# Kernel optimization log

Measured on AMD Instinct MI355X. Metric: run time of the kernel, lower is better.

## Reference

```python
import jax, jax.numpy as jnp
import numpy as np

EMBEDDING_DIM = 512
HEAD_DIM = 64
B, T_NEW, T_CACHE = 8, 1024, 3072
T_TOTAL = T_NEW + T_CACHE


def setup_inputs() -> dict:
    key = jax.random.key(0)
    ks = jax.random.split(key, 6)
    x = jax.random.normal(ks[0], (B, T_NEW, EMBEDDING_DIM), dtype=jnp.float32)
    cache_k = jax.random.normal(ks[1], (B, T_CACHE, HEAD_DIM), dtype=jnp.float32)
    cache_v = jax.random.normal(ks[2], (B, T_CACHE, HEAD_DIM), dtype=jnp.float32)
    # Causal mask rows for the new tokens: cache fully visible, causal among new.
    # Equivalent to tril(ones(T_TOTAL, T_TOTAL))[T_CACHE:, :].
    rows = jnp.arange(T_NEW)[:, None] + T_CACHE  # absolute positions of new tokens
    cols = jnp.arange(T_TOTAL)[None, :]
    mask = (cols <= rows).astype(jnp.int32)  # [T_NEW, T_TOTAL]
    scale = 1.0 / np.sqrt(EMBEDDING_DIM)
    Wq = jax.random.normal(ks[3], (EMBEDDING_DIM, HEAD_DIM), dtype=jnp.float32) * scale
    Wk = jax.random.normal(ks[4], (EMBEDDING_DIM, HEAD_DIM), dtype=jnp.float32) * scale
    Wv = jax.random.normal(ks[5], (EMBEDDING_DIM, HEAD_DIM), dtype=jnp.float32) * scale
    return {"x": x, "mask": mask, "cache_k": cache_k, "cache_v": cache_v,
            "Wq": Wq, "Wk": Wk, "Wv": Wv}


def reference(x, mask, cache_k, cache_v, Wq, Wk, Wv):
    # Projections (nn.Linear with bias=False)
    q = jnp.einsum("btc,cd->btd", x, Wq)  # [B, T_new, D]
    k_new = jnp.einsum("btc,cd->btd", x, Wk)
    v_new = jnp.einsum("btc,cd->btd", x, Wv)
    k = jnp.concatenate([cache_k, k_new], axis=1)  # [B, T_total, D]
    v = jnp.concatenate([cache_v, v_new], axis=1)
    d = k.shape[-1]
    scores = jnp.einsum("btd,bsd->bts", q, k) * (d ** -0.5)  # [B, T_new, T_total]
    T = q.shape[1]
    cur_mask = mask[:T, :k.shape[1]]  # [T_new, T_total]
    scores = jnp.where(cur_mask == 0, jnp.float32(-jnp.inf), scores)
    probs = jax.nn.softmax(scores, axis=-1)
    # Dropout is identity in eval mode (deterministic reference).
    out = jnp.einsum("bts,bsd->btd", probs, v)  # [B, T_new, D]
    return out, k, v
```

## Files before the change

kernel.cpp:

```cpp
#include <hip/hip_runtime.h>

#define NB     8
#define TNEW   1024
#define TCACHE 3072
#define TTOT   4096
#define EMB    512
#define HD     64

typedef __bf16 bf16x8 __attribute__((ext_vector_type(8)));
typedef __bf16 bf16x4 __attribute__((ext_vector_type(4)));
typedef float  f32x4  __attribute__((ext_vector_type(4)));

#define MFMA(a,b,c) __builtin_amdgcn_mfma_f32_16x16x32_bf16((a),(b),(c),0,0,0)

#define GLOAD_LDS16(g, l) \
    __builtin_amdgcn_global_load_lds((const __attribute__((address_space(1))) void*)(g), \
                                     (__attribute__((address_space(3))) void*)(l), 16, 0, 0)

#define QSCALE 0.180336880f

#define WS_WT   0
#define WS_KBF  196608
#define WS_VTB  4390912
#define WS_OP   8585216
#define WS_ML   16973824


__global__ __launch_bounds__(256) void prep(const float* __restrict__ ck,
                                            const float* __restrict__ cv,
                                            const float* __restrict__ Wq,
                                            const float* __restrict__ Wk,
                                            const float* __restrict__ Wv,
                                            float* __restrict__ kout,
                                            float* __restrict__ vout,
                                            __bf16* __restrict__ kb,
                                            __bf16* __restrict__ vtb,
                                            __bf16* __restrict__ wt) {
    __shared__ __bf16 vl[64][72];
    const int blk = blockIdx.x;
    const int tid = threadIdx.x;
    if (blk < 768) {
#pragma unroll
        for (int it = 0; it < 2; ++it) {
            const int i = blk * 256 + tid + it * 196608;
            const int b = i / 49152;
            const int f = i - b * 49152;
            const int s = f >> 4, d = (f & 15) * 4;
            const float4 kd = ((const float4*)ck)[i];
            ((float4*)(kout + (size_t)b * TTOT * HD))[f] = kd;
            bf16x4 k4;
            k4[0] = (__bf16)kd.x; k4[1] = (__bf16)kd.y;
            k4[2] = (__bf16)kd.z; k4[3] = (__bf16)kd.w;
            *(bf16x4*)(kb + (size_t)b * TTOT * HD + s * HD + d) = k4;
        }
    } else if (blk < 1152) {
        const int tb = blk - 768;
        const int b = tb / 48, si = tb - (tb / 48) * 48;
        const int sbase = si * 64;
        const float4* src = (const float4*)(cv + ((size_t)b * TCACHE + sbase) * HD);
        float4* dstf = (float4*)(vout + ((size_t)b * TTOT + sbase) * HD);
#pragma unroll
        for (int k = 0; k < 4; ++k) {
            const int f = tid + 256 * k;
            const int s = f >> 4, d4 = (f & 15) * 4;
            const float4 v = src[f];
            dstf[f] = v;
            bf16x4 t;
            t[0] = (__bf16)v.x; t[1] = (__bf16)v.y;
            t[2] = (__bf16)v.z; t[3] = (__bf16)v.w;
            *(bf16x4*)&vl[s][d4] = t;
        }
        __syncthreads();
        const int d = tid >> 2, sc = tid & 3;
        bf16x8 o0, o1;
#pragma unroll
        for (int i = 0; i < 8; ++i) {
            o0[i] = vl[sc * 16 + i][d];
            o1[i] = vl[sc * 16 + 8 + i][d];
        }
        __bf16* vt = vtb + ((size_t)b * HD + d) * TTOT + sbase + sc * 16;
        *(bf16x8*)vt = o0;
        *(bf16x8*)(vt + 8) = o1;
    } else {
        const int tb = blk - 1152;
        const int m = tb >> 3;
        const int ct = (tb & 7) * 64;
        const float* W = (m == 0) ? Wq : (m == 1) ? Wk : Wv;
        const float4* src = (const float4*)(W + (size_t)ct * HD);
#pragma unroll
        for (int k = 0; k < 4; ++k) {
            const int f = tid + 256 * k;
            const int c = f >> 4, d4 = (f & 15) * 4;
            const float4 v = src[f];
            bf16x4 t;
            t[0] = (__bf16)v.x; t[1] = (__bf16)v.y;
            t[2] = (__bf16)v.z; t[3] = (__bf16)v.w;
            *(bf16x4*)&vl[c][d4] = t;
        }
        __syncthreads();
        const int d = tid >> 2, sc = tid & 3;
        bf16x8 o0, o1;
#pragma unroll
        for (int i = 0; i < 8; ++i) {
            o0[i] = vl[sc * 16 + i][d];
            o1[i] = vl[sc * 16 + 8 + i][d];
        }
        __bf16* wr = wt + (size_t)m * HD * EMB + (size_t)d * EMB + ct + sc * 16;
        *(bf16x8*)wr = o0;
        *(bf16x8*)(wr + 8) = o1;
    }
}

__global__ __launch_bounds__(128) void proj_mfma(const float* __restrict__ x,
                                                 const __bf16* __restrict__ wt,
                                                 __bf16* __restrict__ qb,
                                                 float* __restrict__ kout,
                                                 float* __restrict__ vout,
                                                 __bf16* __restrict__ kb,
                                                 __bf16* __restrict__ vtb) {
    __shared__ __bf16 xs[32][520];
    __shared__ __bf16 vls[2][64][24];
    const int tid = threadIdx.x;
    const int w = tid >> 6, lane = tid & 63;
    const int lo = lane & 15, hi = lane >> 4;
    const int r0 = blockIdx.x * 32 + w * 16;
    const int b = r0 >> 10;
    const int t0r = r0 & (TNEW - 1);

    {
        const float4* xg = (const float4*)(x + (size_t)blockIdx.x * 32 * EMB);
#pragma unroll
        for (int k = 0; k < 32; ++k) {
            const int f = tid + 128 * k;
            const int row = f >> 7, col4 = (f & 127) * 4;
            const float4 v = xg[f];
            bf16x4 t;
            t[0] = (__bf16)v.x; t[1] = (__bf16)v.y;
            t[2] = (__bf16)v.z; t[3] = (__bf16)v.w;
            *(bf16x4*)&xs[row][col4] = t;
        }
    }
    __syncthreads();

    for (int m = 0; m < 3; ++m) {
        const __bf16* wm = wt + (size_t)m * HD * EMB;
        f32x4 acc[4];
#pragma unroll
        for (int n = 0; n < 4; ++n) acc[n] = (f32x4){0.f, 0.f, 0.f, 0.f};
#pragma unroll
        for (int c = 0; c < 16; ++c) {
            const bf16x8 ax = *(const bf16x8*)&xs[w * 16 + lo][c * 32 + hi * 8];
#pragma unroll
            for (int n = 0; n < 4; ++n) {
                const bf16x8 bw = *(const bf16x8*)(wm + (size_t)(n * 16 + lo) * EMB + c * 32 + hi * 8);
                acc[n] = MFMA(ax, bw, acc[n]);
            }
        }
#pragma unroll
        for (int n = 0; n < 4; ++n) {
#pragma unroll
            for (int rr = 0; rr < 4; ++rr) {
                const int grow = r0 + hi * 4 + rr;
                const int t = grow & (TNEW - 1);
                const int d = n * 16 + lo;
                const float val = acc[n][rr];
                if (m == 0) {
                    qb[(size_t)grow * HD + d] = (__bf16)(val * QSCALE);
                } else if (m == 1) {
                    const size_t kv = ((size_t)b * TTOT + TCACHE + t) * HD + d;
                    kout[kv] = val;
                    kb[kv] = (__bf16)val;
                } else {
                    const size_t kv = ((size_t)b * TTOT + TCACHE + t) * HD + d;
                    vout[kv] = val;
                    vls[w][d][hi * 4 + rr] = (__bf16)val;
                }
            }
        }
    }
    __syncthreads();
    bf16x8 v0 = *(const bf16x8*)&vls[w][lane][0];
    bf16x8 v1 = *(const bf16x8*)&vls[w][lane][8];
    __bf16* vt = vtb + ((size_t)b * HD + lane) * TTOT + TCACHE + t0r;
    *(bf16x8*)vt = v0;
    *(bf16x8*)(vt + 8) = v1;
}

#define QB 128
#define NSPLIT 8
__global__ __launch_bounds__(512, 4) void attn_mfma(const __bf16* __restrict__ qb,
                                                    const __bf16* __restrict__ kb,
                                                    const __bf16* __restrict__ vtb,
                                                    __bf16* __restrict__ Opart,
                                                    float* __restrict__ mlpart) {
    __shared__ __align__(16) __bf16 Kt[3][64 * 64];
    __shared__ __align__(16) __bf16 Vts[3][64 * 64];
    __shared__ __align__(16) __bf16 P_lds[8][16][72];

    const int tid = threadIdx.x;
    const int wv = tid >> 6, lane = tid & 63;
    const int lo = lane & 15, hi = lane >> 4;

    const int bid = blockIdx.x;
    const int b = bid & 7;
    const int idx = bid >> 3;
    const int split = idx & 7;
    const int qloc = idx >> 3;
    const int t0 = qloc * QB;
    const int row0 = b * TNEW + t0;

    const int ntiles = (TCACHE + t0 + QB) >> 6;
    const int count = (ntiles - split + 7) >> 3;

    const __bf16* Kb = kb + (size_t)b * TTOT * HD;
    const __bf16* Vb = vtb + (size_t)b * HD * TTOT;

    const int r_sub = lane >> 3;
    const int row_st = wv * 8 + r_sub;
    const int c_st = ((lane & 7) * 16) ^ (r_sub << 4);

#define STAGE(s, bi) do { \
        const char* gk_ = (const char*)Kb + (size_t)((s) + row_st) * 128 + c_st; \
        const char* gv_ = (const char*)Vb + ((size_t)row_st * TTOT + (s)) * 2 + c_st; \
        GLOAD_LDS16(gk_, Kt[bi] + row_st * 64); \
        GLOAD_LDS16(gv_, Vts[bi] + row_st * 64); \
    } while (0)

    const int t0w = t0 + wv * 16;
    const __bf16* Qw = qb + (size_t)(row0 + wv * 16) * HD;
    const bf16x8 aq0 = *(const bf16x8*)(Qw + (size_t)lo * HD + hi * 8);
    const bf16x8 aq1 = *(const bf16x8*)(Qw + (size_t)lo * HD + 32 + hi * 8);

    f32x4 o[4];
    float mg = -1e30f, lg = 0.f;
#pragma unroll
    for (int n = 0; n < 4; ++n) o[n] = (f32x4){0.f, 0.f, 0.f, 0.f};

    STAGE(split * 64, 0);
    if (count > 1) {
        STAGE(split * 64 + 512, 1);
        asm volatile("s_waitcnt vmcnt(2)" ::: "memory");
    } else {
        asm volatile("s_waitcnt vmcnt(0)" ::: "memory");
    }
    __builtin_amdgcn_s_barrier();
    __builtin_amdgcn_sched_barrier(0);

    const int sw = (lo & 7) << 3;

    int s0 = split * 64;
    int buf = 0;
    for (int it = 0; it < count; ++it, s0 += NSPLIT * 64) {
        const __bf16* Kl = Kt[buf];
        const __bf16* Vl = Vts[buf];

        bf16x8 bk[4][2], bv[4][2];
#pragma unroll
        for (int kg = 0; kg < 4; ++kg) {
            const int kr = (kg * 16 + lo) * 64;
            bk[kg][0] = *(const bf16x8*)(Kl + kr + ((hi * 8) ^ sw));
            bk[kg][1] = *(const bf16x8*)(Kl + kr + ((32 + hi * 8) ^ sw));
        }
#pragma unroll
        for (int n = 0; n < 4; ++n) {
            const int vr = (n * 16 + lo) * 64;
            bv[n][0] = *(const bf16x8*)(Vl + vr + ((hi * 8) ^ sw));
            bv[n][1] = *(const bf16x8*)(Vl + vr + ((32 + hi * 8) ^ sw));
        }

        const f32x4 z = (f32x4){0.f, 0.f, 0.f, 0.f};
        f32x4 sc[4];
#pragma unroll
        for (int kg = 0; kg < 4; ++kg) {
            sc[kg] = MFMA(bk[kg][0], aq0, z);
            sc[kg] = MFMA(bk[kg][1], aq1, sc[kg]);
        }

        if (s0 + 63 > TCACHE + t0w) {
            const int lim = TCACHE + t0w + lo;
#pragma unroll
            for (int kg = 0; kg < 4; ++kg)
#pragma unroll
                for (int rr = 0; rr < 4; ++rr)
                    if (s0 + kg * 16 + hi * 4 + rr > lim) sc[kg][rr] = -1e30f;
        }

        f32x4 mx = sc[0];
        mx = (f32x4){fmaxf(mx[0], sc[1][0]), fmaxf(mx[1], sc[1][1]),
                     fmaxf(mx[2], sc[1][2]), fmaxf(mx[3], sc[1][3])};
        mx = (f32x4){fmaxf(mx[0], sc[2][0]), fmaxf(mx[1], sc[2][1]),
                     fmaxf(mx[2], sc[2][2]), fmaxf(mx[3], sc[2][3])};
        mx = (f32x4){fmaxf(mx[0], sc[3][0]), fmaxf(mx[1], sc[3][1]),
                     fmaxf(mx[2], sc[3][2]), fmaxf(mx[3], sc[3][3])};
        float mt = fmaxf(fmaxf(mx[0], mx[1]), fmaxf(mx[2], mx[3]));
        mt = fmaxf(mt, __shfl_xor(mt, 16));
        mt = fmaxf(mt, __shfl_xor(mt, 32));

        if (__any(mt > mg + 8.0f)) {
            const float mn = fmaxf(mg, mt);
            const float corr = exp2f(mg - mn);
            lg *= corr;
            mg = mn;
            float cb[4];
#pragma unroll
            for (int rr = 0; rr < 4; ++rr) cb[rr] = __shfl(corr, hi * 4 + rr);
#pragma unroll
            for (int n = 0; n < 4; ++n)
#pragma unroll
                for (int rr = 0; rr < 4; ++rr) o[n][rr] *= cb[rr];
        }

        float ps = 0.f;
#pragma unroll
        for (int kg = 0; kg < 4; ++kg) {
            const float e0 = exp2f(sc[kg][0] - mg);
            const float e1 = exp2f(sc[kg][1] - mg);
            const float e2 = exp2f(sc[kg][2] - mg);
            const float e3 = exp2f(sc[kg][3] - mg);
            ps += (e0 + e1) + (e2 + e3);
            bf16x4 pk;
            pk[0] = (__bf16)e0; pk[1] = (__bf16)e1;
            pk[2] = (__bf16)e2; pk[3] = (__bf16)e3;
            *(bf16x4*)&P_lds[wv][lo][kg * 16 + hi * 4] = pk;
        }
        ps += __shfl_xor(ps, 16);
        ps += __shfl_xor(ps, 32);
        lg += ps;
        asm volatile("" ::: "memory");

        const bf16x8 ap0 = *(const bf16x8*)&P_lds[wv][lo][hi * 8];
        const bf16x8 ap1 = *(const bf16x8*)&P_lds[wv][lo][32 + hi * 8];
#pragma unroll
        for (int n = 0; n < 4; ++n) o[n] = MFMA(ap0, bv[n][0], o[n]);
#pragma unroll
        for (int n = 0; n < 4; ++n) o[n] = MFMA(ap1, bv[n][1], o[n]);
        asm volatile("" ::: "memory");

        if (it + 2 < count) {
            int nb = buf + 2; if (nb >= 3) nb -= 3;
            STAGE(s0 + 2 * NSPLIT * 64, nb);
        }
        if (it + 1 < count) {
            if (it + 2 < count) { asm volatile("s_waitcnt vmcnt(2)" ::: "memory"); }
            else                { asm volatile("s_waitcnt vmcnt(0)" ::: "memory"); }
            __builtin_amdgcn_s_barrier();
            __builtin_amdgcn_sched_barrier(0);
        }
        buf = (buf == 2) ? 0 : buf + 1;
    }
#undef STAGE

    __bf16* Ow = Opart + ((size_t)split * (NB * TNEW) + row0 + wv * 16) * HD;
#pragma unroll
    for (int n = 0; n < 4; ++n)
#pragma unroll
        for (int rr = 0; rr < 4; ++rr)
            Ow[(size_t)(hi * 4 + rr) * HD + n * 16 + lo] = (__bf16)o[n][rr];
    if (hi == 0) {
        float* mlw = mlpart + ((size_t)split * (NB * TNEW) + row0 + wv * 16) * 2;
        mlw[lo * 2]     = mg;
        mlw[lo * 2 + 1] = lg;
    }
}

__global__ __launch_bounds__(256) void combine(const __bf16* __restrict__ Opart,
                                               const float* __restrict__ mlpart,
                                               float* __restrict__ out) {
    const int e = blockIdx.x * 256 + threadIdx.x;
    const int lane = threadIdx.x & 63;
    const int row = e >> 6, d = e & 63;
    const float2 ml2 = *(const float2*)&mlpart[(((size_t)(lane & 7)) * (NB * TNEW) + row) * 2];
    float mf = -1e30f;
#pragma unroll
    for (int s = 0; s < NSPLIT; ++s) mf = fmaxf(mf, __shfl(ml2.x, s));
    float lf = 0.f, acc = 0.f;
#pragma unroll
    for (int s = 0; s < NSPLIT; ++s) {
        const float ms = __shfl(ml2.x, s);
        const float ls = __shfl(ml2.y, s);
        const float f = exp2f(ms - mf);
        lf += ls * f;
        acc += (float)Opart[((size_t)s * (NB * TNEW) + row) * HD + d] * f;
    }
    out[e] = acc / lf;
}

extern "C" void kernel_launch(void* const* d_in, const int* in_sizes, int n_in,
                              void* d_out, int out_size, void* d_ws, size_t ws_size,
                              hipStream_t stream) {
    (void)in_sizes; (void)n_in; (void)out_size; (void)ws_size;
    const float* x  = (const float*)d_in[0];
    const float* ck = (const float*)d_in[2];
    const float* cv = (const float*)d_in[3];
    const float* Wq = (const float*)d_in[4];
    const float* Wk = (const float*)d_in[5];
    const float* Wv = (const float*)d_in[6];

    float* out  = (float*)d_out;
    float* kout = out + (size_t)NB * TNEW * HD;
    float* vout = kout + (size_t)NB * TTOT * HD;

    char* ws = (char*)d_ws;
    __bf16* wt  = (__bf16*)(ws + WS_WT);
    __bf16* kbf = (__bf16*)(ws + WS_KBF);
    __bf16* vtb = (__bf16*)(ws + WS_VTB);
    __bf16* Op  = (__bf16*)(ws + WS_OP);
    float*  ml  = (float*)(ws + WS_ML);
    __bf16* qb  = (__bf16*)d_out;

    prep<<<dim3(1176), dim3(256), 0, stream>>>(ck, cv, Wq, Wk, Wv, kout, vout, kbf, vtb, wt);
    proj_mfma<<<dim3(256), dim3(128), 0, stream>>>(x, wt, qb, kout, vout, kbf, vtb);
    attn_mfma<<<dim3(512), dim3(512), 0, stream>>>(qb, kbf, vtb, Op, ml);
    combine<<<dim3(2048), dim3(256), 0, stream>>>(Op, ml, out);
}
```

Measured before the change: 50.09 us.

## Keep P in registers by permuting V^T token layout; raise attention occupancy

The V^T buffer is now written with a permuted token order within each 64-token tile. This lets the exponentiated scores from the QK MFMA output be packed directly into the A operand of the PV MFMA, with no round trip through LDS. The P_lds buffer and its stores and loads are removed. K and V fragments are now loaded just before use instead of all up front, and launch bounds rise to 6 waves per SIMD, which should lower register pressure and raise occupancy. The risks are the narrower 8-byte V^T stores, possible spills under the tighter register budget, and correctness depending on the K-dimension permutation matching exactly.

Result: no change. 50.39 us (+0.6%).

```diff
diff --git a/kernel.cpp b/kernel.cpp
--- a/kernel.cpp
+++ b/kernel.cpp
@@ -72,15 +72,14 @@
         }
         __syncthreads();
         const int d = tid >> 2, sc = tid & 3;
-        bf16x8 o0, o1;
-#pragma unroll
-        for (int i = 0; i < 8; ++i) {
-            o0[i] = vl[sc * 16 + i][d];
-            o1[i] = vl[sc * 16 + 8 + i][d];
-        }
-        __bf16* vt = vtb + ((size_t)b * HD + d) * TTOT + sbase + sc * 16;
-        *(bf16x8*)vt = o0;
-        *(bf16x8*)(vt + 8) = o1;
+        __bf16* vt = vtb + ((size_t)b * HD + d) * TTOT + sbase + (sc >> 1) * 32 + (sc & 1) * 4;
+#pragma unroll
+        for (int t4 = 0; t4 < 4; ++t4) {
+            bf16x4 o;
+#pragma unroll
+            for (int c = 0; c < 4; ++c) o[c] = vl[sc * 16 + t4 * 4 + c][d];
+            *(bf16x4*)(vt + t4 * 8) = o;
+        }
     } else {
         const int tb = blk - 1152;
         const int m = tb >> 3;
@@ -179,23 +178,29 @@
         }
     }
     __syncthreads();
-    bf16x8 v0 = *(const bf16x8*)&vls[w][lane][0];
-    bf16x8 v1 = *(const bf16x8*)&vls[w][lane][8];
-    __bf16* vt = vtb + ((size_t)b * HD + lane) * TTOT + TCACHE + t0r;
-    *(bf16x8*)vt = v0;
-    *(bf16x8*)(vt + 8) = v1;
+    {
+        const int tb4 = TCACHE + (t0r & ~63);
+        const int m4 = (t0r >> 4) & 3;
+        __bf16* vt = vtb + ((size_t)b * HD + lane) * TTOT + tb4 + (m4 >> 1) * 32 + (m4 & 1) * 4;
+#pragma unroll
+        for (int t4 = 0; t4 < 4; ++t4) {
+            bf16x4 o;
+#pragma unroll
+            for (int c = 0; c < 4; ++c) o[c] = vls[w][lane][t4 * 4 + c];
+            *(bf16x4*)(vt + t4 * 8) = o;
+        }
+    }
 }
 
 #define QB 128
 #define NSPLIT 8
-__global__ __launch_bounds__(512, 4) void attn_mfma(const __bf16* __restrict__ qb,
+__global__ __launch_bounds__(512, 6) void attn_mfma(const __bf16* __restrict__ qb,
                                                     const __bf16* __restrict__ kb,
                                                     const __bf16* __restrict__ vtb,
                                                     __bf16* __restrict__ Opart,
                                                     float* __restrict__ mlpart) {
     __shared__ __align__(16) __bf16 Kt[3][64 * 64];
     __shared__ __align__(16) __bf16 Vts[3][64 * 64];
-    __shared__ __align__(16) __bf16 P_lds[8][16][72];
 
     const int tid = threadIdx.x;
     const int wv = tid >> 6, lane = tid & 63;
@@ -254,26 +259,15 @@
         const __bf16* Kl = Kt[buf];
         const __bf16* Vl = Vts[buf];
 
-        bf16x8 bk[4][2], bv[4][2];
+        const f32x4 z = (f32x4){0.f, 0.f, 0.f, 0.f};
+        f32x4 sc[4];
 #pragma unroll
         for (int kg = 0; kg < 4; ++kg) {
             const int kr = (kg * 16 + lo) * 64;
-            bk[kg][0] = *(const bf16x8*)(Kl + kr + ((hi * 8) ^ sw));
-            bk[kg][1] = *(const bf16x8*)(Kl + kr + ((32 + hi * 8) ^ sw));
-        }
-#pragma unroll
-        for (int n = 0; n < 4; ++n) {
-            const int vr = (n * 16 + lo) * 64;
-            bv[n][0] = *(const bf16x8*)(Vl + vr + ((hi * 8) ^ sw));
-            bv[n][1] = *(const bf16x8*)(Vl + vr + ((32 + hi * 8) ^ sw));
-        }
-
-        const f32x4 z = (f32x4){0.f, 0.f, 0.f, 0.f};
-        f32x4 sc[4];
-#pragma unroll
-        for (int kg = 0; kg < 4; ++kg) {
-            sc[kg] = MFMA(bk[kg][0], aq0, z);
-            sc[kg] = MFMA(bk[kg][1], aq1, sc[kg]);
+            const bf16x8 bk0 = *(const bf16x8*)(Kl + kr + ((hi * 8) ^ sw));
+            const bf16x8 bk1 = *(const bf16x8*)(Kl + kr + ((32 + hi * 8) ^ sw));
+            sc[kg] = MFMA(bk0, aq0, z);
+            sc[kg] = MFMA(bk1, aq1, sc[kg]);
         }
 
         if (s0 + 63 > TCACHE + t0w) {
@@ -310,31 +304,41 @@
                 for (int rr = 0; rr < 4; ++rr) o[n][rr] *= cb[rr];
         }
 
+        float e[4][4];
         float ps = 0.f;
 #pragma unroll
         for (int kg = 0; kg < 4; ++kg) {
-            const float e0 = exp2f(sc[kg][0] - mg);
-            const float e1 = exp2f(sc[kg][1] - mg);
-            const float e2 = exp2f(sc[kg][2] - mg);
-            const float e3 = exp2f(sc[kg][3] - mg);
-            ps += (e0 + e1) + (e2 + e3);
-            bf16x4 pk;
-            pk[0] = (__bf16)e0; pk[1] = (__bf16)e1;
-            pk[2] = (__bf16)e2; pk[3] = (__bf16)e3;
-            *(bf16x4*)&P_lds[wv][lo][kg * 16 + hi * 4] = pk;
+#pragma unroll
+            for (int rr = 0; rr < 4; ++rr) {
+                e[kg][rr] = exp2f(sc[kg][rr] - mg);
+                ps += e[kg][rr];
+            }
         }
         ps += __shfl_xor(ps, 16);
         ps += __shfl_xor(ps, 32);
         lg += ps;
-        asm volatile("" ::: "memory");
-
-        const bf16x8 ap0 = *(const bf16x8*)&P_lds[wv][lo][hi * 8];
-        const bf16x8 ap1 = *(const bf16x8*)&P_lds[wv][lo][32 + hi * 8];
-#pragma unroll
-        for (int n = 0; n < 4; ++n) o[n] = MFMA(ap0, bv[n][0], o[n]);
-#pragma unroll
-        for (int n = 0; n < 4; ++n) o[n] = MFMA(ap1, bv[n][1], o[n]);
-        asm volatile("" ::: "memory");
+
+        bf16x8 ap0, ap1;
+#pragma unroll
+        for (int rr = 0; rr < 4; ++rr) {
+            ap0[rr]     = (__bf16)e[0][rr];
+            ap0[4 + rr] = (__bf16)e[1][rr];
+            ap1[rr]     = (__bf16)e[2][rr];
+            ap1[4 + rr] = (__bf16)e[3][rr];
+        }
+
+#pragma unroll
+        for (int n = 0; n < 4; ++n) {
+            const int vr = (n * 16 + lo) * 64;
+            const bf16x8 bv0 = *(const bf16x8*)(Vl + vr + ((hi * 8) ^ sw));
+            o[n] = MFMA(ap0, bv0, o[n]);
+        }
+#pragma unroll
+        for (int n = 0; n < 4; ++n) {
+            const int vr = (n * 16 + lo) * 64;
+            const bf16x8 bv1 = *(const bf16x8*)(Vl + vr + ((32 + hi * 8) ^ sw));
+            o[n] = MFMA(ap1, bv1, o[n]);
+        }
 
         if (it + 2 < count) {
             int nb = buf + 2; if (nb >= 3) nb -= 3;
```
